# Performance work log

Measured on AMD Instinct MI355X. Metric: run time of the kernel, lower is better.

The kernel has to match this reference:

```python
import jax, jax.numpy as jnp
import numpy as np

# TT-linear: in_features=1024 -> out_features=4096
IN_DIMS = (8, 8, 4, 4)      # m1..m4, prod = 1024
OUT_DIMS = (8, 8, 8, 8)     # n1..n4, prod = 4096
RANKS = (1, 16, 16, 16, 1)  # r0..r4
IN_FEATURES = 1024
OUT_FEATURES = 4096
BATCH, SEQ = 4, 1024


def _init_core(key, shape):
    # uniform(-1,1)/sqrt(fan_in-ish), matching the original's uniform-style init scale
    fan = shape[0] * shape[1]
    return (2.0 * jax.random.uniform(key, shape, dtype=jnp.float32) - 1.0) / np.sqrt(fan).astype(np.float32)


def setup_inputs() -> dict:
    key = jax.random.key(0)
    ks = jax.random.split(key, 6)
    x = jax.random.normal(ks[0], (BATCH, SEQ, IN_FEATURES), dtype=jnp.float32)
    core0 = _init_core(ks[1], (1, 8, 8, 16))    # [r0, m1, n1, r1]
    core1 = _init_core(ks[2], (16, 8, 8, 16))   # [r1, m2, n2, r2]
    core2 = _init_core(ks[3], (16, 4, 8, 16))   # [r2, m3, n3, r3]
    core3 = _init_core(ks[4], (16, 4, 8, 1))    # [r3, m4, n4, r4]
    bias = (2.0 * jax.random.uniform(ks[5], (OUT_FEATURES,), dtype=jnp.float32) - 1.0) / np.sqrt(OUT_FEATURES).astype(np.float32)
    return {"x": x, "core0": core0, "core1": core1, "core2": core2, "core3": core3, "bias": bias}


def reference(x, core0, core1, core2, core3, bias):
    lead = x.shape[:-1]
    # split the feature axis into TT input factors: [T, m1, m2, m3, m4]
    t = x.reshape((-1,) + IN_DIMS)
    c0 = core0[0]        # [m1, n1, r1]   (boundary rank r0 = 1 squeezed)
    c3 = core3[..., 0]   # [r3, m4, n4]   (boundary rank r4 = 1 squeezed)
    # sequential TT core chain: absorb one m_k, emit one n_k per step
    t = jnp.einsum('tijkl,ixp->tjklxp', t, c0)      # [T, m2,m3,m4, n1, r1]
    t = jnp.einsum('tjklxp,pjyq->tklxyq', t, core1)  # [T, m3,m4, n1,n2, r2]
    t = jnp.einsum('tklxyq,qkzr->tlxyzr', t, core2)  # [T, m4, n1,n2,n3, r3]
    t = jnp.einsum('tlxyzr,rlw->txyzw', t, c3)       # [T, n1,n2,n3,n4]
    y = t.reshape(lead + (OUT_FEATURES,)) + bias
    return y
```

## Files before the change

### kernel.cpp

```cpp
#include <hip/hip_runtime.h>
#include <hip/hip_bf16.h>
#include <cstdint>


typedef __bf16 bf16x8 __attribute__((ext_vector_type(8)));
typedef float f32x4 __attribute__((ext_vector_type(4)));

__device__ __forceinline__ void g2lds16(const void* g, void* l) {
    __builtin_amdgcn_global_load_lds(
        (const __attribute__((address_space(1))) void*)g,
        (__attribute__((address_space(3))) void*)l,
        16, 0, 0);
}

__global__ __launch_bounds__(256) void prep(
    const float* __restrict__ x, __bf16* __restrict__ xb,
    const float* __restrict__ c0, const float* __restrict__ c1,
    const float* __restrict__ c2, const float* __restrict__ c3,
    __bf16* __restrict__ wt) {
    const int b = blockIdx.x;
    const int t = threadIdx.x;
    if (b < 2048) {
        const int i = (b * 256 + t) * 8;
        float4 a0 = *(const float4*)(x + i);
        float4 a1 = *(const float4*)(x + i + 4);
        bf16x8 o;
        o[0] = (__bf16)a0.x; o[1] = (__bf16)a0.y; o[2] = (__bf16)a0.z; o[3] = (__bf16)a0.w;
        o[4] = (__bf16)a1.x; o[5] = (__bf16)a1.y; o[6] = (__bf16)a1.z; o[7] = (__bf16)a1.w;
        *(bf16x8*)(xb + i) = o;
        return;
    }
    __shared__ float t12[4][16];
    __shared__ float t123[4][512];
    __shared__ float c3s[512];
    #pragma unroll
    for (int i = t; i < 512; i += 256) c3s[i] = c3[i];
    const int s = t >> 6;
    const int lane = t & 63;
    const int g = (b - 2048) * 4 + s;
    const int m1 = g >> 9, n1 = (g >> 6) & 7, m2 = (g >> 3) & 7, n2 = g & 7;
    __syncthreads();
    if (lane < 16) {
        const int r2 = lane;
        float sum = 0.f;
        #pragma unroll
        for (int r1 = 0; r1 < 16; ++r1)
            sum += c0[(m1 * 8 + n1) * 16 + r1] * c1[((r1 * 8 + m2) * 8 + n2) * 16 + r2];
        t12[s][r2] = sum;
    }
    __syncthreads();
    #pragma unroll
    for (int idx = lane; idx < 512; idx += 64) {
        const int m3 = idx >> 7, n3 = (idx >> 4) & 7, r3 = idx & 15;
        float sum = 0.f;
        #pragma unroll
        for (int r2 = 0; r2 < 16; ++r2)
            sum += t12[s][r2] * c2[((r2 * 4 + m3) * 8 + n3) * 16 + r3];
        t123[s][(m3 * 8 + n3) * 16 + r3] = sum;
    }
    __syncthreads();
    const int n3 = lane >> 3, n4 = lane & 7;
    const int n = ((n1 * 8 + n2) * 8 + n3) * 8 + n4;
    const int kbase = (m1 * 8 + m2) * 16;
    float v[16];
    #pragma unroll
    for (int e = 0; e < 16; ++e) v[e] = 0.f;
    #pragma unroll
    for (int m3 = 0; m3 < 4; ++m3) {
        #pragma unroll
        for (int r3 = 0; r3 < 16; ++r3) {
            const float tv = t123[s][(m3 * 8 + n3) * 16 + r3];
            #pragma unroll
            for (int m4 = 0; m4 < 4; ++m4)
                v[m3 * 4 + m4] += tv * c3s[(r3 * 4 + m4) * 8 + n4];
        }
    }
    bf16x8 lo, hi;
    #pragma unroll
    for (int e = 0; e < 8; ++e) { lo[e] = (__bf16)v[e]; hi[e] = (__bf16)v[8 + e]; }
    *(bf16x8*)(wt + (size_t)n * 1024 + kbase)     = lo;
    *(bf16x8*)(wt + (size_t)n * 1024 + kbase + 8) = hi;
}


#define SCHED() __builtin_amdgcn_sched_barrier(0)
#define BAR()  do { SCHED(); __builtin_amdgcn_s_barrier(); SCHED(); } while (0)
#define WAITVM(n) do { SCHED(); asm volatile("s_waitcnt vmcnt(" #n ")"); SCHED(); } while (0)

__global__ __launch_bounds__(512, 2) void tt_gemm(
    const __bf16* __restrict__ A, const __bf16* __restrict__ B,
    const float* __restrict__ bias, float* __restrict__ C) {
    constexpr int K = 1024, N = 4096;
    constexpr int NKT = 16;
    __shared__ __bf16 sA[2][2][256 * 32];
    __shared__ __bf16 sB[2][2][256 * 32];
    const int t = threadIdx.x;
    const int lane = t & 63;
    const int wave = t >> 6;
    const int wm = (wave >> 2) * 128;
    const int wn = (wave & 3) * 64;
    const int l15 = lane & 15, lh = lane >> 4;
    const int cOff = ((lh ^ ((l15 >> 1) & 3)) << 4);

    const int xcd = blockIdx.x & 7;
    const int lid = blockIdx.x >> 3;
    const int bm = ((xcd >> 2) * 8 + (lid & 7)) * 256;
    const int bn = ((xcd & 3) * 4 + (lid >> 3)) * 256;

    const int c0i = t, c1i = t + 512;
    const int r0 = c0i >> 2, r1 = c1i >> 2;
    const int lc0 = (c0i & 3) ^ ((r0 >> 1) & 3);
    const int lc1 = (c1i & 3) ^ ((r1 >> 1) & 3);
    const __bf16* a0p = A + (size_t)(bm + r0) * K + lc0 * 8;
    const __bf16* a1p = A + (size_t)(bm + r1) * K + lc1 * 8;
    const __bf16* b0p = B + (size_t)(bn + r0) * K + lc0 * 8;
    const __bf16* b1p = B + (size_t)(bn + r1) * K + lc1 * 8;

#define ST_A(kt, ks) do { \
    g2lds16(a0p + (size_t)(kt) * 64 + (ks) * 32, (char*)&sA[(kt) & 1][ks][0] + c0i * 16); \
    g2lds16(a1p + (size_t)(kt) * 64 + (ks) * 32, (char*)&sA[(kt) & 1][ks][0] + c1i * 16); } while (0)
#define ST_B(kt, ks) do { \
    g2lds16(b0p + (size_t)(kt) * 64 + (ks) * 32, (char*)&sB[(kt) & 1][ks][0] + c0i * 16); \
    g2lds16(b1p + (size_t)(kt) * 64 + (ks) * 32, (char*)&sB[(kt) & 1][ks][0] + c1i * 16); } while (0)
#define LDA(dst, fi, ks) dst = *(const bf16x8*)((const char*)&sA[slot][ks][0] + (wm + (fi) * 16 + l15) * 64 + cOff)
#define LDB(dst, ni, ks) dst = *(const bf16x8*)((const char*)&sB[slot][ks][0] + (wn + (ni) * 16 + l15) * 64 + cOff)
#define MFMA16(base, afr) do { \
    __builtin_amdgcn_s_setprio(1); \
    _Pragma("unroll") \
    for (int mi = 0; mi < 4; ++mi) \
        _Pragma("unroll") \
        for (int ni = 0; ni < 4; ++ni) \
            acc[(base) + mi][ni] = __builtin_amdgcn_mfma_f32_16x16x32_bf16( \
                afr[mi], bb[ni], acc[(base) + mi][ni], 0, 0, 0); \
    __builtin_amdgcn_s_setprio(0); } while (0)

    f32x4 acc[8][4] = {};

    ST_A(0, 0); ST_B(0, 0);
    ST_A(0, 1); ST_B(0, 1);
    ST_A(1, 0); ST_B(1, 0);
    WAITVM(8);
    BAR();

    #pragma unroll 1
    for (int kt = 0; kt < NKT; ++kt) {
        const int slot = kt & 1;
        bf16x8 aL[4], aH[4], bb[4];
        #pragma unroll
        for (int mi = 0; mi < 4; ++mi) LDA(aL[mi], mi, 0);
        #pragma unroll
        for (int ni = 0; ni < 4; ++ni) LDB(bb[ni], ni, 0);
        if (kt < NKT - 1) ST_A(kt + 1, 1);
        BAR();
        MFMA16(0, aL);
        BAR();
        #pragma unroll
        for (int mi = 0; mi < 4; ++mi) LDA(aH[mi], 4 + mi, 0);
        if (kt < NKT - 1) ST_B(kt + 1, 1);
        BAR();
        MFMA16(4, aH);
        if (kt < NKT - 1) { WAITVM(8); } else { WAITVM(0); }
        BAR();
        #pragma unroll
        for (int mi = 0; mi < 4; ++mi) LDA(aL[mi], mi, 1);
        #pragma unroll
        for (int ni = 0; ni < 4; ++ni) LDB(bb[ni], ni, 1);
        if (kt < NKT - 2) ST_A(kt + 2, 0);
        BAR();
        MFMA16(0, aL);
        BAR();
        #pragma unroll
        for (int mi = 0; mi < 4; ++mi) LDA(aH[mi], 4 + mi, 1);
        if (kt < NKT - 2) ST_B(kt + 2, 0);
        BAR();
        MFMA16(4, aH);
        if (kt < NKT - 2)      { WAITVM(8); }
        else if (kt == NKT - 2) { WAITVM(4); }
        BAR();
    }

    float bv[4];
    #pragma unroll
    for (int ni = 0; ni < 4; ++ni) bv[ni] = bias[bn + wn + ni * 16 + l15];
    #pragma unroll
    for (int mi = 0; mi < 8; ++mi) {
        #pragma unroll
        for (int r = 0; r < 4; ++r) {
            const int row = bm + wm + mi * 16 + lh * 4 + r;
            float* crow = C + (size_t)row * N + bn + wn + l15;
            #pragma unroll
            for (int ni = 0; ni < 4; ++ni)
                crow[ni * 16] = acc[mi][ni][r] + bv[ni];
        }
    }
#undef ST_A
#undef ST_B
#undef LDA
#undef LDB
#undef MFMA16
}

extern "C" void kernel_launch(void* const* d_in, const int* in_sizes, int n_in,
                              void* d_out, int out_size, void* d_ws, size_t ws_size,
                              hipStream_t stream) {
    const float* x    = (const float*)d_in[0];
    const float* c0   = (const float*)d_in[1];
    const float* c1   = (const float*)d_in[2];
    const float* c2   = (const float*)d_in[3];
    const float* c3   = (const float*)d_in[4];
    const float* bias = (const float*)d_in[5];
    float* out = (float*)d_out;

    __bf16* xb = (__bf16*)d_ws;
    __bf16* wt = xb + (size_t)4096 * 1024;

    prep<<<3072, 256, 0, stream>>>(x, xb, c0, c1, c2, c3, wt);
    tt_gemm<<<256, 512, 0, stream>>>(xb, wt, bias, out);
}
```

Measured before the change: 135.9 us.

## Shrink GEMM tile to 256x128 with triple-buffered K=32 pipeline

Halves the N tile from 256 to 128, which doubles the grid to 512 blocks, and reduces per-wave accumulators from 8x4 to 8x2 fragments. The K step drops to 32 per iteration with a three-slot LDS ring that prefetches two steps ahead, and launch bounds now request 4 blocks per CU. The goal is more occupancy and better load balance across CUs. The cost is lower arithmetic intensity per tile, more A-tile reloads from global memory, and more barriers per unit of work.

```diff
diff --git a/kernel.cpp b/kernel.cpp
--- a/kernel.cpp
+++ b/kernel.cpp
@@ -87,117 +87,101 @@
 #define BAR()  do { SCHED(); __builtin_amdgcn_s_barrier(); SCHED(); } while (0)
 #define WAITVM(n) do { SCHED(); asm volatile("s_waitcnt vmcnt(" #n ")"); SCHED(); } while (0)
 
-__global__ __launch_bounds__(512, 2) void tt_gemm(
+__global__ __launch_bounds__(512, 4) void tt_gemm(
     const __bf16* __restrict__ A, const __bf16* __restrict__ B,
     const float* __restrict__ bias, float* __restrict__ C) {
     constexpr int K = 1024, N = 4096;
-    constexpr int NKT = 16;
-    __shared__ __bf16 sA[2][2][256 * 32];
-    __shared__ __bf16 sB[2][2][256 * 32];
+    constexpr int NKT = 32;
+    __shared__ __bf16 sA[3][256 * 32];
+    __shared__ __bf16 sB[3][128 * 32];
     const int t = threadIdx.x;
     const int lane = t & 63;
     const int wave = t >> 6;
     const int wm = (wave >> 2) * 128;
-    const int wn = (wave & 3) * 64;
+    const int wn = (wave & 3) * 32;
     const int l15 = lane & 15, lh = lane >> 4;
     const int cOff = ((lh ^ ((l15 >> 1) & 3)) << 4);
 
     const int xcd = blockIdx.x & 7;
     const int lid = blockIdx.x >> 3;
-    const int bm = ((xcd >> 2) * 8 + (lid & 7)) * 256;
-    const int bn = ((xcd & 3) * 4 + (lid >> 3)) * 256;
+    const int bmo = ((xcd >> 2) * 8 + (lid & 7)) * 256;
+    const int bno = ((xcd & 3) * 8 + (lid >> 3)) * 128;
 
     const int c0i = t, c1i = t + 512;
-    const int r0 = c0i >> 2, r1 = c1i >> 2;
-    const int lc0 = (c0i & 3) ^ ((r0 >> 1) & 3);
-    const int lc1 = (c1i & 3) ^ ((r1 >> 1) & 3);
-    const __bf16* a0p = A + (size_t)(bm + r0) * K + lc0 * 8;
-    const __bf16* a1p = A + (size_t)(bm + r1) * K + lc1 * 8;
-    const __bf16* b0p = B + (size_t)(bn + r0) * K + lc0 * 8;
-    const __bf16* b1p = B + (size_t)(bn + r1) * K + lc1 * 8;
-
-#define ST_A(kt, ks) do { \
-    g2lds16(a0p + (size_t)(kt) * 64 + (ks) * 32, (char*)&sA[(kt) & 1][ks][0] + c0i * 16); \
-    g2lds16(a1p + (size_t)(kt) * 64 + (ks) * 32, (char*)&sA[(kt) & 1][ks][0] + c1i * 16); } while (0)
-#define ST_B(kt, ks) do { \
-    g2lds16(b0p + (size_t)(kt) * 64 + (ks) * 32, (char*)&sB[(kt) & 1][ks][0] + c0i * 16); \
-    g2lds16(b1p + (size_t)(kt) * 64 + (ks) * 32, (char*)&sB[(kt) & 1][ks][0] + c1i * 16); } while (0)
-#define LDA(dst, fi, ks) dst = *(const bf16x8*)((const char*)&sA[slot][ks][0] + (wm + (fi) * 16 + l15) * 64 + cOff)
-#define LDB(dst, ni, ks) dst = *(const bf16x8*)((const char*)&sB[slot][ks][0] + (wn + (ni) * 16 + l15) * 64 + cOff)
-#define MFMA16(base, afr) do { \
+    const int rA0 = c0i >> 2, rA1 = c1i >> 2;
+    const int lcA0 = (c0i & 3) ^ ((rA0 >> 1) & 3);
+    const int lcA1 = (c1i & 3) ^ ((rA1 >> 1) & 3);
+    const int rB = t >> 2;
+    const int lcB = (t & 3) ^ ((rB >> 1) & 3);
+    const __bf16* a0p = A + (size_t)(bmo + rA0) * K + lcA0 * 8;
+    const __bf16* a1p = A + (size_t)(bmo + rA1) * K + lcA1 * 8;
+    const __bf16* bp  = B + (size_t)(bno + rB)  * K + lcB * 8;
+
+#define ST_A(kt, sl) do { \
+    g2lds16(a0p + (size_t)(kt) * 32, (char*)&sA[sl][0] + c0i * 16); \
+    g2lds16(a1p + (size_t)(kt) * 32, (char*)&sA[sl][0] + c1i * 16); } while (0)
+#define ST_B(kt, sl) \
+    g2lds16(bp + (size_t)(kt) * 32, (char*)&sB[sl][0] + t * 16)
+#define LDA(dst, fi) dst = *(const bf16x8*)((const char*)&sA[s0][0] + (wm + (fi) * 16 + l15) * 64 + cOff)
+#define LDB(dst, ni) dst = *(const bf16x8*)((const char*)&sB[s0][0] + (wn + (ni) * 16 + l15) * 64 + cOff)
+#define MFMA8(base, afr) do { \
     __builtin_amdgcn_s_setprio(1); \
     _Pragma("unroll") \
     for (int mi = 0; mi < 4; ++mi) \
         _Pragma("unroll") \
-        for (int ni = 0; ni < 4; ++ni) \
+        for (int ni = 0; ni < 2; ++ni) \
             acc[(base) + mi][ni] = __builtin_amdgcn_mfma_f32_16x16x32_bf16( \
                 afr[mi], bb[ni], acc[(base) + mi][ni], 0, 0, 0); \
     __builtin_amdgcn_s_setprio(0); } while (0)
 
-    f32x4 acc[8][4] = {};
+    f32x4 acc[8][2] = {};
 
     ST_A(0, 0); ST_B(0, 0);
-    ST_A(0, 1); ST_B(0, 1);
-    ST_A(1, 0); ST_B(1, 0);
-    WAITVM(8);
+    ST_A(1, 1); ST_B(1, 1);
+    WAITVM(3);
     BAR();
 
     #pragma unroll 1
     for (int kt = 0; kt < NKT; ++kt) {
-        const int slot = kt & 1;
-        bf16x8 aL[4], aH[4], bb[4];
-        #pragma unroll
-        for (int mi = 0; mi < 4; ++mi) LDA(aL[mi], mi, 0);
-        #pragma unroll
-        for (int ni = 0; ni < 4; ++ni) LDB(bb[ni], ni, 0);
-        if (kt < NKT - 1) ST_A(kt + 1, 1);
-        BAR();
-        MFMA16(0, aL);
-        BAR();
-        #pragma unroll
-        for (int mi = 0; mi < 4; ++mi) LDA(aH[mi], 4 + mi, 0);
-        if (kt < NKT - 1) ST_B(kt + 1, 1);
-        BAR();
-        MFMA16(4, aH);
-        if (kt < NKT - 1) { WAITVM(8); } else { WAITVM(0); }
-        BAR();
-        #pragma unroll
-        for (int mi = 0; mi < 4; ++mi) LDA(aL[mi], mi, 1);
-        #pragma unroll
-        for (int ni = 0; ni < 4; ++ni) LDB(bb[ni], ni, 1);
-        if (kt < NKT - 2) ST_A(kt + 2, 0);
-        BAR();
-        MFMA16(0, aL);
-        BAR();
-        #pragma unroll
-        for (int mi = 0; mi < 4; ++mi) LDA(aH[mi], 4 + mi, 1);
-        if (kt < NKT - 2) ST_B(kt + 2, 0);
-        BAR();
-        MFMA16(4, aH);
-        if (kt < NKT - 2)      { WAITVM(8); }
-        else if (kt == NKT - 2) { WAITVM(4); }
-        BAR();
-    }
-
-    float bv[4];
-    #pragma unroll
-    for (int ni = 0; ni < 4; ++ni) bv[ni] = bias[bn + wn + ni * 16 + l15];
+        const int s0 = kt % 3;
+        const int s2 = (kt + 2) % 3;
+        bf16x8 aL[4], aH[4], bb[2];
+        #pragma unroll
+        for (int mi = 0; mi < 4; ++mi) LDA(aL[mi], mi);
+        #pragma unroll
+        for (int ni = 0; ni < 2; ++ni) LDB(bb[ni], ni);
+        if (kt < NKT - 2) ST_A(kt + 2, s2);
+        BAR();
+        MFMA8(0, aL);
+        BAR();
+        #pragma unroll
+        for (int mi = 0; mi < 4; ++mi) LDA(aH[mi], 4 + mi);
+        if (kt < NKT - 2) ST_B(kt + 2, s2);
+        BAR();
+        MFMA8(4, aH);
+        if (kt < NKT - 2)       { WAITVM(3); }
+        else if (kt == NKT - 2) { WAITVM(0); }
+        BAR();
+    }
+
+    float bv[2];
+    #pragma unroll
+    for (int ni = 0; ni < 2; ++ni) bv[ni] = bias[bno + wn + ni * 16 + l15];
     #pragma unroll
     for (int mi = 0; mi < 8; ++mi) {
         #pragma unroll
         for (int r = 0; r < 4; ++r) {
-            const int row = bm + wm + mi * 16 + lh * 4 + r;
-            float* crow = C + (size_t)row * N + bn + wn + l15;
-            #pragma unroll
-            for (int ni = 0; ni < 4; ++ni)
-                crow[ni * 16] = acc[mi][ni][r] + bv[ni];
+            const int row = bmo + wm + mi * 16 + lh * 4 + r;
+            float* crow = C + (size_t)row * N + bno + wn + l15;
+            crow[0]  = acc[mi][0][r] + bv[0];
+            crow[16] = acc[mi][1][r] + bv[1];
         }
     }
 #undef ST_A
 #undef ST_B
 #undef LDA
 #undef LDB
-#undef MFMA16
+#undef MFMA8
 }
 
 extern "C" void kernel_launch(void* const* d_in, const int* in_sizes, int n_in,
@@ -215,5 +199,5 @@
     __bf16* wt = xb + (size_t)4096 * 1024;
 
     prep<<<3072, 256, 0, stream>>>(x, xb, c0, c1, c2, c3, wt);
-    tt_gemm<<<256, 512, 0, stream>>>(xb, wt, bias, out);
-}
+    tt_gemm<<<512, 512, 0, stream>>>(xb, wt, bias, out);
+}
```

New measurement: 137.4 us. No clear change (+1.1%).
